# Kernel optimization log

Measured on AMD Instinct MI355X. Metric: run time of the kernel, lower is better.

## Reference

```python
import jax, jax.numpy as jnp
import numpy as np
from jax.ops import segment_sum, segment_max, segment_min

N_NODES = 200000
N_HE = 100000     # number of hyperedges (nets)
NNZ = 1000000     # number of pins (node,hyperedge) incidences
F_RAW = 29        # raw node features; +2 fake_pos +1 ismacro = 32 = num_features
PIN_D = 4
C = 64            # nhid (heads = 1)
N_MACRO = 512
NUM_CLASSES = 1
SLOPE = 0.1


def _lrelu(v):
    return jnp.where(v >= 0, v, SLOPE * v)


def setup_inputs() -> dict:
    key = jax.random.key(0)
    ks = jax.random.split(key, 16)
    x = jax.random.normal(ks[0], (N_NODES, F_RAW), jnp.float32)
    fake_pos = jax.random.uniform(ks[1], (N_NODES, 2), dtype=jnp.float32)
    node_idx = jax.random.randint(ks[2], (NNZ,), 0, N_NODES)
    he_idx = jax.random.randint(ks[3], (NNZ,), 0, N_HE)
    edge_index = jnp.stack([node_idx, he_idx]).astype(jnp.int32)
    pin_feature = jax.random.normal(ks[4], (NNZ, PIN_D), jnp.float32)
    macro_index = jax.random.randint(ks[5], (N_MACRO,), 0, N_NODES).astype(jnp.int32)
    F_IN = F_RAW + 3

    def lin(k, fi, fo):
        return (jax.random.normal(k, (fi, fo), jnp.float32) / np.float32(np.sqrt(fi)))

    W1 = lin(ks[6], F_IN, C); b1 = jnp.zeros((C,), jnp.float32)
    Wpin = lin(ks[7], PIN_D, C)
    att = jax.random.normal(ks[8], (2 * C,), jnp.float32) / np.float32(np.sqrt(2 * C))
    Wpost = lin(ks[9], 4 * C, C); bpost = jnp.zeros((C,), jnp.float32)
    Wm1 = lin(ks[10], 2 * C, C); bm1 = jnp.zeros((C,), jnp.float32)
    Wm2 = lin(ks[11], C, C // 2); bm2 = jnp.zeros((C // 2,), jnp.float32)
    Wm3 = lin(ks[12], C // 2, NUM_CLASSES); bm3 = jnp.zeros((NUM_CLASSES,), jnp.float32)
    return dict(x=x, fake_pos=fake_pos, edge_index=edge_index, pin_feature=pin_feature,
                macro_index=macro_index, W1=W1, b1=b1, Wpin=Wpin, att=att,
                Wpost=Wpost, bpost=bpost, Wm1=Wm1, bm1=bm1, Wm2=Wm2, bm2=bm2,
                Wm3=Wm3, bm3=bm3)


def _forward(x, fake_pos, edge_index, pin_feature, macro_index,
             W1, b1, Wpin, att, Wpost, bpost, Wm1, bm1, Wm2, bm2, Wm3, bm3):
    node_idx = edge_index[0]
    he_idx = edge_index[1]

    ismacro = jnp.zeros((N_NODES, 1), x.dtype).at[macro_index].set(1.0)
    h = jnp.concatenate([x, fake_pos, ismacro], axis=-1)  # (N, 32)

    xl = h @ W1 + b1                                      # (N, C) node embedding
    pin_m = pin_feature @ Wpin                            # (NNZ, C) pin embedding

    # node -> hyperedge aggregation (mean over incident pins)
    msg_ne = xl[node_idx] + pin_m                         # (NNZ, C)
    deg_e = segment_sum(jnp.ones((NNZ,), x.dtype), he_idx, num_segments=N_HE)
    e_feat = segment_sum(msg_ne, he_idx, num_segments=N_HE) / jnp.maximum(deg_e, 1.0)[:, None]

    # attention over incident hyperedges, softmax per node
    e_g = e_feat[he_idx]                                  # (NNZ, C)
    a_raw = _lrelu(jnp.concatenate([xl[node_idx], e_g], axis=-1) @ att)  # (NNZ,)
    m = segment_max(a_raw, node_idx, num_segments=N_NODES)
    m = jnp.where(jnp.isfinite(m), m, 0.0)
    ex = jnp.exp(a_raw - m[node_idx])
    den = segment_sum(ex, node_idx, num_segments=N_NODES)
    alpha = ex / (den[node_idx] + 1e-16)

    # hyperedge -> node: PNA multi-aggregation of attention-weighted messages
    msg = e_g * alpha[:, None]                            # (NNZ, C)
    deg_n = segment_sum(jnp.ones((NNZ,), x.dtype), node_idx, num_segments=N_NODES)
    deg_c = jnp.maximum(deg_n, 1.0)[:, None]
    s = segment_sum(msg, node_idx, num_segments=N_NODES)
    mean = s / deg_c
    mx = segment_max(msg, node_idx, num_segments=N_NODES)
    mx = jnp.where(deg_n[:, None] > 0, mx, 0.0)
    mn = segment_min(msg, node_idx, num_segments=N_NODES)
    mn = jnp.where(deg_n[:, None] > 0, mn, 0.0)
    sq = segment_sum(msg * msg, node_idx, num_segments=N_NODES) / deg_c
    std = jnp.sqrt(jnp.maximum(sq - mean * mean, 0.0) + 1e-12)

    pna = jnp.concatenate([mean, mx, mn, std], axis=-1) @ Wpost + bpost  # (N, C)
    hx = _lrelu(pna)

    # masked global-mean pools (single graph: batch is all zeros)
    pooled = jnp.concatenate([hx[macro_index].mean(0), hx.mean(0)])[None, :]  # (1, 2C)

    z = _lrelu(pooled @ Wm1 + bm1)
    z = _lrelu(z @ Wm2 + bm2)
    return z @ Wm3 + bm3                                  # (1, num_classes)


def reference(x, fake_pos, edge_index, pin_feature, macro_index,
              W1, b1, Wpin, att, Wpost, bpost, Wm1, bm1, Wm2, bm2, Wm3, bm3):
    return _forward(x, fake_pos, edge_index, pin_feature, macro_index,
                    W1, b1, Wpin, att, Wpost, bpost, Wm1, bm1, Wm2, bm2, Wm3, bm3)
```

## Files before the change

### kernel.cpp

```cpp
#include <hip/hip_runtime.h>
#include <math.h>

#define N_NODES 200000
#define N_HE    100000
#define NNZ     1000000
#define F_RAW   29
#define N_MACRO 512
#define SLOPE   0.1f
#define L_TOTAL (N_NODES + N_HE)
#define NB_SCAN 293

typedef __attribute__((ext_vector_type(8))) short bf16x8;
typedef __attribute__((ext_vector_type(4))) float f32x4;

__device__ __forceinline__ float lrelu(float v) { return v >= 0.f ? v : SLOPE * v; }
__device__ __forceinline__ float bf2f(unsigned short u) { return __uint_as_float(((unsigned)u) << 16); }
__device__ __forceinline__ unsigned short f2bf(float f) {
    unsigned u = __float_as_uint(f);
    unsigned r = u + 0x7FFFu + ((u >> 16) & 1u);
    return (unsigned short)(r >> 16);
}
__device__ __forceinline__ float bflo(unsigned u) { return __uint_as_float(u << 16); }
__device__ __forceinline__ float bfhi(unsigned u) { return __uint_as_float(u & 0xffff0000u); }

__global__ __launch_bounds__(256) void fill_f32(float* p, long long n, float v) {
    long long i = (long long)blockIdx.x * blockDim.x + threadIdx.x;
    long long st = (long long)gridDim.x * blockDim.x;
    for (; i < n; i += st) p[i] = v;
}

__global__ __launch_bounds__(256) void k_ismacro(const int* __restrict__ mi,
                                                 float* __restrict__ ismacro, int* __restrict__ mcount) {
    int i = blockIdx.x * blockDim.x + threadIdx.x;
    if (i < N_MACRO) {
        ismacro[mi[i]] = 1.0f;
        atomicAdd(&mcount[mi[i]], 1);
    }
}

__global__ __launch_bounds__(64) void k_va(const float* __restrict__ W1, const float* __restrict__ b1,
                                           const float* __restrict__ att, float* __restrict__ va) {
    int t = threadIdx.x;
    if (t < 32) {
        float a = 0.f;
        for (int c = 0; c < 64; c++) a += W1[t * 64 + c] * att[c];
        va[t] = a;
    } else if (t == 32) {
        float a = 0.f;
        for (int c = 0; c < 64; c++) a += b1[c] * att[c];
        va[32] = a;
    }
}

__global__ __launch_bounds__(256) void k_h(
    const float* __restrict__ x, const float* __restrict__ fp,
    const float* __restrict__ ismacro, const float* __restrict__ va,
    unsigned short* __restrict__ h, float* __restrict__ xn_att)
{
    const int lane = threadIdx.x & 63;
    const int half = lane >> 5, k = lane & 31;
    int wid = (blockIdx.x * blockDim.x + threadIdx.x) >> 6;
    int nw = (gridDim.x * blockDim.x) >> 6;
    float vak = va[k];
    float c0 = va[32];
    for (int base = wid * 2; base < N_NODES; base += nw * 2) {
        int n = base + half;
        float v;
        if (k < 29)       v = x[(size_t)n * F_RAW + k];
        else if (k == 29) v = fp[2 * n];
        else if (k == 30) v = fp[2 * n + 1];
        else              v = ismacro[n];
        h[(size_t)n * 32 + k] = f2bf(v);
        float r = v * vak;
        #pragma unroll
        for (int o = 16; o > 0; o >>= 1) r += __shfl_xor(r, o, 32);
        if (k == 0) xn_att[n] = r + c0;
    }
}

__global__ __launch_bounds__(256) void k_count(
    const int* __restrict__ nidx, const int* __restrict__ hidx,
    int* __restrict__ cnt, int* __restrict__ rank_n, int* __restrict__ rank_e)
{
    int i = blockIdx.x * blockDim.x + threadIdx.x;
    int st = gridDim.x * blockDim.x;
    for (int p = i; p < NNZ; p += st) {
        rank_n[p] = atomicAdd(&cnt[nidx[p]], 1);
        rank_e[p] = atomicAdd(&cnt[N_NODES + hidx[p]], 1);
    }
}

__global__ __launch_bounds__(256) void k_scan1(const int* __restrict__ cnt,
                                               int* __restrict__ row_ptr, int* __restrict__ partials)
{
    __shared__ int sA[256], sB[256];
    const int t = threadIdx.x;
    const int base = blockIdx.x * 1024 + t * 4;
    int v0 = base + 0 < L_TOTAL ? cnt[base + 0] : 0;
    int v1 = base + 1 < L_TOTAL ? cnt[base + 1] : 0;
    int v2 = base + 2 < L_TOTAL ? cnt[base + 2] : 0;
    int v3 = base + 3 < L_TOTAL ? cnt[base + 3] : 0;
    sA[t] = v0 + v1 + v2 + v3;
    __syncthreads();
    int* src = sA; int* dst = sB;
    for (int off = 1; off < 256; off <<= 1) {
        int v = src[t];
        if (t >= off) v += src[t - off];
        dst[t] = v;
        __syncthreads();
        int* tmp = src; src = dst; dst = tmp;
    }
    int excl = t > 0 ? src[t - 1] : 0;
    if (base + 0 < L_TOTAL) row_ptr[base + 0] = excl;
    if (base + 1 < L_TOTAL) row_ptr[base + 1] = excl + v0;
    if (base + 2 < L_TOTAL) row_ptr[base + 2] = excl + v0 + v1;
    if (base + 3 < L_TOTAL) row_ptr[base + 3] = excl + v0 + v1 + v2;
    if (t == 255) partials[blockIdx.x] = src[255];
}

__global__ __launch_bounds__(512) void k_scan2(int* __restrict__ partials)
{
    __shared__ int sA[512], sB[512];
    const int t = threadIdx.x;
    sA[t] = t < NB_SCAN ? partials[t] : 0;
    __syncthreads();
    int* src = sA; int* dst = sB;
    for (int off = 1; off < 512; off <<= 1) {
        int v = src[t];
        if (t >= off) v += src[t - off];
        dst[t] = v;
        __syncthreads();
        int* tmp = src; src = dst; dst = tmp;
    }
    if (t < NB_SCAN) partials[t] = t > 0 ? src[t - 1] : 0;
    if (t == 0) partials[NB_SCAN] = src[511];
}

__global__ __launch_bounds__(256) void k_scan3(int* __restrict__ row_ptr, const int* __restrict__ partials)
{
    const int base = blockIdx.x * 1024 + threadIdx.x * 4;
    int add = partials[blockIdx.x];
    #pragma unroll
    for (int k = 0; k < 4; k++)
        if (base + k < L_TOTAL) row_ptr[base + k] += add;
    if (blockIdx.x == 0 && threadIdx.x == 0) row_ptr[L_TOTAL] = partials[NB_SCAN];
}

__global__ __launch_bounds__(256) void k_scatter(
    const int* __restrict__ nidx, const int* __restrict__ hidx,
    const int* __restrict__ row_ptr,
    const int* __restrict__ rank_n, const int* __restrict__ rank_e,
    const float4* __restrict__ pf4, int* __restrict__ csr, ushort4* __restrict__ pfh)
{
    int i = blockIdx.x * blockDim.x + threadIdx.x;
    int st = gridDim.x * blockDim.x;
    for (int p = i; p < NNZ; p += st) {
        int n = nidx[p], e = hidx[p];
        csr[row_ptr[n] + rank_n[p]] = e;
        int pe = row_ptr[N_NODES + e] + rank_e[p];
        csr[pe] = n;
        float4 q = pf4[p];
        ushort4 r;
        r.x = f2bf(q.x); r.y = f2bf(q.y); r.z = f2bf(q.z); r.w = f2bf(q.w);
        pfh[pe - NNZ] = r;
    }
}

__global__ __launch_bounds__(256) void k_he_agg(
    const int* __restrict__ row_ptr, const int* __restrict__ csr,
    const ushort4* __restrict__ pfh,
    const float* __restrict__ W1, const float* __restrict__ Wpin,
    const float* __restrict__ b1, const float* __restrict__ att,
    const unsigned short* __restrict__ h,
    unsigned short* __restrict__ e_feat, float* __restrict__ e_att)
{
    __shared__ float sW1[32 * 64];
    __shared__ float sWp[4 * 64];
    __shared__ float sb1[64];
    for (int i = threadIdx.x; i < 32 * 64; i += 256) sW1[i] = W1[i];
    for (int i = threadIdx.x; i < 4 * 64; i += 256) sWp[i] = Wpin[i];
    if (threadIdx.x < 64) sb1[threadIdx.x] = b1[threadIdx.x];
    __syncthreads();
    const int lane = threadIdx.x & 63;
    const int g  = lane >> 4;
    const int gl = lane & 15;
    float att2 = att[64 + lane];
    int wid = (blockIdx.x * blockDim.x + threadIdx.x) >> 6;
    int nw = (gridDim.x * blockDim.x) >> 6;
    for (int e = wid; e < N_HE; e += nw) {
        int start = row_ptr[N_NODES + e];
        int deg = row_ptr[N_NODES + e + 1] - start;
        float hx = 0.f, hy = 0.f;
        {
            int t = g;
            for (; t + 4 < deg; t += 8) {
                int n0 = csr[start + t];
                int n1 = csr[start + t + 4];
                unsigned u0 = ((const unsigned*)&h[(size_t)n0 * 32])[gl];
                unsigned u1 = ((const unsigned*)&h[(size_t)n1 * 32])[gl];
                hx += bflo(u0) + bflo(u1);
                hy += bfhi(u0) + bfhi(u1);
            }
            for (; t < deg; t += 4) {
                int n = csr[start + t];
                unsigned u = ((const unsigned*)&h[(size_t)n * 32])[gl];
                hx += bflo(u); hy += bfhi(u);
            }
        }
        hx += __shfl_xor(hx, 16); hy += __shfl_xor(hy, 16);
        hx += __shfl_xor(hx, 32); hy += __shfl_xor(hy, 32);
        float p0 = 0.f, p1 = 0.f, p2 = 0.f, p3 = 0.f;
        for (int t = lane; t < deg; t += 64) {
            ushort4 r = pfh[start - NNZ + t];
            p0 += bf2f(r.x); p1 += bf2f(r.y); p2 += bf2f(r.z); p3 += bf2f(r.w);
        }
        #pragma unroll
        for (int o = 32; o > 0; o >>= 1) {
            p0 += __shfl_xor(p0, o, 64); p1 += __shfl_xor(p1, o, 64);
            p2 += __shfl_xor(p2, o, 64); p3 += __shfl_xor(p3, o, 64);
        }
        float acc = (float)deg * sb1[lane]
                  + p0 * sWp[lane] + p1 * sWp[64 + lane]
                  + p2 * sWp[128 + lane] + p3 * sWp[192 + lane];
        #pragma unroll
        for (int kk = 0; kk < 16; kk++) {
            float hvx = __shfl(hx, kk, 64);
            float hvy = __shfl(hy, kk, 64);
            acc += hvx * sW1[(2 * kk) * 64 + lane] + hvy * sW1[(2 * kk + 1) * 64 + lane];
        }
        float d = (float)(deg > 0 ? deg : 1);
        float v = acc / d;
        e_feat[(size_t)e * 64 + lane] = f2bf(v);
        float r = v * att2;
        #pragma unroll
        for (int o = 32; o > 0; o >>= 1) r += __shfl_down(r, o, 64);
        if (lane == 0) e_att[e] = r;
    }
}

__global__ __launch_bounds__(256, 4) void k_fused(
    const int* __restrict__ row_ptr, const int* __restrict__ csr,
    const float* __restrict__ xn_att, const float* __restrict__ e_att,
    const unsigned short* __restrict__ e_feat,
    const float* __restrict__ Wpost, const float* __restrict__ bpost,
    const int* __restrict__ mcount,
    float* __restrict__ sum_all, float* __restrict__ sum_mac)
{
    __shared__ __align__(16) unsigned short scat[16 * 264];
    const int lane = threadIdx.x & 63;
    const int wave = threadIdx.x >> 6;
    const int half = lane >> 5;
    const int c2   = lane & 31;
    const int quad = lane >> 4;
    const int nn   = lane & 15;
    bf16x8 wfrag[8];
    #pragma unroll
    for (int s = 0; s < 8; s++) {
        bf16x8 w;
        #pragma unroll
        for (int j = 0; j < 8; j++)
            w[j] = (short)f2bf(Wpost[(size_t)(32 * s + quad * 8 + j) * 64 + wave * 16 + nn]);
        wfrag[s] = w;
    }
    float bias = bpost[wave * 16 + nn];
    float pool = 0.f, pmac = 0.f;
    const int nbatches = N_NODES / 16;
    for (int b = blockIdx.x; b < nbatches; b += gridDim.x) {
        const int base = b * 16;
        __syncthreads();
        for (int i = 0; i < 4; i++) {
            int j = wave * 4 + i;
            int n = base + j;
            int start = row_ptr[n];
            int deg = row_ptr[n + 1] - start;
            float xn = xn_att[n];
            float sw = 0.f;
            float sx = 0.f, sy = 0.f, qx = 0.f, qy = 0.f;
            float mxx = -INFINITY, mxy = -INFINITY, mnx = INFINITY, mny = INFINITY;
            int t = half;
            for (; t + 2 < deg; t += 4) {
                int e0 = csr[start + t];
                int e1 = csr[start + t + 2];
                float w0 = __expf(lrelu(xn + e_att[e0]));
                float w1 = __expf(lrelu(xn + e_att[e1]));
                unsigned u0 = ((const unsigned*)&e_feat[(size_t)e0 * 64])[c2];
                unsigned u1 = ((const unsigned*)&e_feat[(size_t)e1 * 64])[c2];
                float v0x = bflo(u0) * w0, v0y = bfhi(u0) * w0;
                float v1x = bflo(u1) * w1, v1y = bfhi(u1) * w1;
                sw += w0 + w1;
                sx += v0x + v1x; sy += v0y + v1y;
                qx += v0x * v0x + v1x * v1x; qy += v0y * v0y + v1y * v1y;
                mxx = fmaxf(mxx, fmaxf(v0x, v1x)); mxy = fmaxf(mxy, fmaxf(v0y, v1y));
                mnx = fminf(mnx, fminf(v0x, v1x)); mny = fminf(mny, fminf(v0y, v1y));
            }
            for (; t < deg; t += 2) {
                int e = csr[start + t];
                float w = __expf(lrelu(xn + e_att[e]));
                unsigned u = ((const unsigned*)&e_feat[(size_t)e * 64])[c2];
                float vx = bflo(u) * w, vy = bfhi(u) * w;
                sw += w; sx += vx; sy += vy; qx += vx * vx; qy += vy * vy;
                mxx = fmaxf(mxx, vx); mxy = fmaxf(mxy, vy);
                mnx = fminf(mnx, vx); mny = fminf(mny, vy);
            }
            sw  += __shfl_xor(sw, 32);
            sx  += __shfl_xor(sx, 32);  sy += __shfl_xor(sy, 32);
            qx  += __shfl_xor(qx, 32);  qy += __shfl_xor(qy, 32);
            mxx = fmaxf(mxx, __shfl_xor(mxx, 32)); mxy = fmaxf(mxy, __shfl_xor(mxy, 32));
            mnx = fminf(mnx, __shfl_xor(mnx, 32)); mny = fminf(mny, __shfl_xor(mny, 32));
            float invD = 1.f / (sw + 1e-16f);
            float dc = (float)(deg > 0 ? deg : 1);
            float meanx = sx * invD / dc, meany = sy * invD / dc;
            float sqmx = qx * invD * invD / dc, sqmy = qy * invD * invD / dc;
            float stdx = sqrtf(fmaxf(sqmx - meanx * meanx, 0.f) + 1e-12f);
            float stdy = sqrtf(fmaxf(sqmy - meany * meany, 0.f) + 1e-12f);
            ushort2* row = (ushort2*)&scat[j * 264];
            if (half == 0) {
                ushort2 a; a.x = f2bf(meanx); a.y = f2bf(meany);
                row[c2] = a;
                ushort2 bmax; bmax.x = f2bf(deg > 0 ? mxx * invD : 0.f);
                bmax.y = f2bf(deg > 0 ? mxy * invD : 0.f);
                row[32 + c2] = bmax;
            } else {
                ushort2 bmin; bmin.x = f2bf(deg > 0 ? mnx * invD : 0.f);
                bmin.y = f2bf(deg > 0 ? mny * invD : 0.f);
                row[64 + c2] = bmin;
                ushort2 bstd; bstd.x = f2bf(stdx); bstd.y = f2bf(stdy);
                row[96 + c2] = bstd;
            }
        }
        __syncthreads();
        f32x4 acc = {0.f, 0.f, 0.f, 0.f};
        #pragma unroll
        for (int s = 0; s < 8; s++) {
            bf16x8 a = *(const bf16x8*)&scat[nn * 264 + 32 * s + quad * 8];
            acc = __builtin_amdgcn_mfma_f32_16x16x32_bf16(a, wfrag[s], acc, 0, 0, 0);
        }
        int4 mc4 = *(const int4*)&mcount[base + 4 * quad];
        float h0 = lrelu(acc[0] + bias);
        float h1 = lrelu(acc[1] + bias);
        float h2 = lrelu(acc[2] + bias);
        float h3 = lrelu(acc[3] + bias);
        pool += h0 + h1 + h2 + h3;
        pmac += (float)mc4.x * h0 + (float)mc4.y * h1 + (float)mc4.z * h2 + (float)mc4.w * h3;
    }
    pool += __shfl_xor(pool, 16); pool += __shfl_xor(pool, 32);
    pmac += __shfl_xor(pmac, 16); pmac += __shfl_xor(pmac, 32);
    if (quad == 0) {
        atomicAdd(&sum_all[wave * 16 + nn], pool);
        atomicAdd(&sum_mac[wave * 16 + nn], pmac);
    }
}

__global__ __launch_bounds__(256) void k_final(
    const float* __restrict__ sum_all, const float* __restrict__ sum_mac,
    const float* __restrict__ Wm1, const float* __restrict__ bm1,
    const float* __restrict__ Wm2, const float* __restrict__ bm2,
    const float* __restrict__ Wm3, const float* __restrict__ bm3,
    float* __restrict__ out)
{
    __shared__ float spool[128];
    __shared__ float z1[64];
    __shared__ float z2[32];
    if (threadIdx.x < 64) {
        spool[threadIdx.x]      = sum_mac[threadIdx.x] / (float)N_MACRO;
        spool[64 + threadIdx.x] = sum_all[threadIdx.x] / (float)N_NODES;
    }
    __syncthreads();
    if (threadIdx.x < 64) {
        int j = threadIdx.x;
        float a = bm1[j];
        #pragma unroll 4
        for (int k = 0; k < 128; k++) a += spool[k] * Wm1[k * 64 + j];
        z1[j] = lrelu(a);
    }
    __syncthreads();
    if (threadIdx.x < 32) {
        int j = threadIdx.x;
        float a = bm2[j];
        #pragma unroll 4
        for (int k = 0; k < 64; k++) a += z1[k] * Wm2[k * 32 + j];
        z2[j] = lrelu(a);
    }
    __syncthreads();
    if (threadIdx.x == 0) {
        float a = bm3[0];
        #pragma unroll
        for (int k = 0; k < 32; k++) a += z2[k] * Wm3[k];
        out[0] = a;
    }
}

extern "C" void kernel_launch(void* const* d_in, const int* in_sizes, int n_in,
                              void* d_out, int out_size, void* d_ws, size_t ws_size,
                              hipStream_t stream)
{
    const float* x        = (const float*)d_in[0];
    const float* fake_pos = (const float*)d_in[1];
    const int*   edge     = (const int*)d_in[2];
    const float* pinf     = (const float*)d_in[3];
    const int*   macro    = (const int*)d_in[4];
    const float* W1    = (const float*)d_in[5];
    const float* b1    = (const float*)d_in[6];
    const float* Wpin  = (const float*)d_in[7];
    const float* att   = (const float*)d_in[8];
    const float* Wpost = (const float*)d_in[9];
    const float* bpost = (const float*)d_in[10];
    const float* Wm1   = (const float*)d_in[11];
    const float* bm1   = (const float*)d_in[12];
    const float* Wm2   = (const float*)d_in[13];
    const float* bm2   = (const float*)d_in[14];
    const float* Wm3   = (const float*)d_in[15];
    const float* bm3   = (const float*)d_in[16];
    float* out = (float*)d_out;

    float* ws = (float*)d_ws;
    float*    ismacro = ws;
    float*    sum_all = ws + 200000;
    float*    sum_mac = ws + 200064;
    int*      mcount  = (int*)(ws + 200128);
    int*      cnt     = (int*)(ws + 400128);
    int*      row_ptr  = (int*)(ws + 700128);
    int*      partials = (int*)(ws + 1000132);
    float*    va       = ws + 1000432;
    int*      rank_n   = (int*)(ws + 1000472);
    int*      rank_e   = (int*)(ws + 2000472);
    int*      csr      = (int*)(ws + 3000472);
    ushort4*  pfh      = (ushort4*)(ws + 5000472);
    float*    e_att    = ws + 7000472;
    float*    xn_att   = ws + 7100472;
    unsigned short* h      = (unsigned short*)(ws + 7300472);
    unsigned short* e_feat = (unsigned short*)(ws + 10500472);

    const int* nidx = edge;
    const int* hidx = edge + NNZ;

    fill_f32<<<1024, 256, 0, stream>>>(ws, 700128LL, 0.f);
    k_ismacro<<<2, 256, 0, stream>>>(macro, ismacro, mcount);
    k_count<<<2048, 256, 0, stream>>>(nidx, hidx, cnt, rank_n, rank_e);
    k_va<<<1, 64, 0, stream>>>(W1, b1, att, va);
    k_h<<<2048, 256, 0, stream>>>(x, fake_pos, ismacro, va, h, xn_att);
    k_scan1<<<NB_SCAN, 256, 0, stream>>>(cnt, row_ptr, partials);
    k_scan2<<<1, 512, 0, stream>>>(partials);
    k_scan3<<<NB_SCAN, 256, 0, stream>>>(row_ptr, partials);
    k_scatter<<<2048, 256, 0, stream>>>(nidx, hidx, row_ptr, rank_n, rank_e,
                                        (const float4*)pinf, csr, pfh);
    k_he_agg<<<2048, 256, 0, stream>>>(row_ptr, csr, pfh, W1, Wpin, b1, att, h, e_feat, e_att);
    k_fused<<<2048, 256, 0, stream>>>(row_ptr, csr, xn_att, e_att, e_feat, Wpost, bpost,
                                      mcount, sum_all, sum_mac);
    k_final<<<1, 256, 0, stream>>>(sum_all, sum_mac, Wm1, bm1, Wm2, bm2, Wm3, bm3, out);
}
```

Baseline: 499.3 us.

## Merge small setup kernels and pack hyperedge pin records with node ids

```diff
diff --git a/kernel.cpp b/kernel.cpp
--- a/kernel.cpp
+++ b/kernel.cpp
@@ -29,64 +29,37 @@
     for (; i < n; i += st) p[i] = v;
 }
 
-__global__ __launch_bounds__(256) void k_ismacro(const int* __restrict__ mi,
-                                                 float* __restrict__ ismacro, int* __restrict__ mcount) {
-    int i = blockIdx.x * blockDim.x + threadIdx.x;
-    if (i < N_MACRO) {
-        ismacro[mi[i]] = 1.0f;
-        atomicAdd(&mcount[mi[i]], 1);
-    }
-}
-
-__global__ __launch_bounds__(64) void k_va(const float* __restrict__ W1, const float* __restrict__ b1,
-                                           const float* __restrict__ att, float* __restrict__ va) {
-    int t = threadIdx.x;
-    if (t < 32) {
-        float a = 0.f;
-        for (int c = 0; c < 64; c++) a += W1[t * 64 + c] * att[c];
-        va[t] = a;
-    } else if (t == 32) {
-        float a = 0.f;
-        for (int c = 0; c < 64; c++) a += b1[c] * att[c];
-        va[32] = a;
-    }
-}
-
-__global__ __launch_bounds__(256) void k_h(
-    const float* __restrict__ x, const float* __restrict__ fp,
-    const float* __restrict__ ismacro, const float* __restrict__ va,
-    unsigned short* __restrict__ h, float* __restrict__ xn_att)
-{
-    const int lane = threadIdx.x & 63;
-    const int half = lane >> 5, k = lane & 31;
-    int wid = (blockIdx.x * blockDim.x + threadIdx.x) >> 6;
-    int nw = (gridDim.x * blockDim.x) >> 6;
-    float vak = va[k];
-    float c0 = va[32];
-    for (int base = wid * 2; base < N_NODES; base += nw * 2) {
-        int n = base + half;
-        float v;
-        if (k < 29)       v = x[(size_t)n * F_RAW + k];
-        else if (k == 29) v = fp[2 * n];
-        else if (k == 30) v = fp[2 * n + 1];
-        else              v = ismacro[n];
-        h[(size_t)n * 32 + k] = f2bf(v);
-        float r = v * vak;
-        #pragma unroll
-        for (int o = 16; o > 0; o >>= 1) r += __shfl_xor(r, o, 32);
-        if (k == 0) xn_att[n] = r + c0;
-    }
-}
-
-__global__ __launch_bounds__(256) void k_count(
+__global__ __launch_bounds__(256) void k_pre(
+    const int* __restrict__ mi, float* __restrict__ ismacro, int* __restrict__ mcount,
+    const float* __restrict__ W1, const float* __restrict__ b1,
+    const float* __restrict__ att, float* __restrict__ va,
     const int* __restrict__ nidx, const int* __restrict__ hidx,
     int* __restrict__ cnt, int* __restrict__ rank_n, int* __restrict__ rank_e)
 {
-    int i = blockIdx.x * blockDim.x + threadIdx.x;
-    int st = gridDim.x * blockDim.x;
-    for (int p = i; p < NNZ; p += st) {
-        rank_n[p] = atomicAdd(&cnt[nidx[p]], 1);
-        rank_e[p] = atomicAdd(&cnt[N_NODES + hidx[p]], 1);
+    if (blockIdx.x == 0) {
+        int t = threadIdx.x;
+        if (t < 32) {
+            float a = 0.f;
+            for (int c = 0; c < 64; c++) a += W1[t * 64 + c] * att[c];
+            va[t] = a;
+        } else if (t == 32) {
+            float a = 0.f;
+            for (int c = 0; c < 64; c++) a += b1[c] * att[c];
+            va[32] = a;
+        }
+    } else if (blockIdx.x <= 2) {
+        int i = (blockIdx.x - 1) * 256 + threadIdx.x;
+        if (i < N_MACRO) {
+            ismacro[mi[i]] = 1.0f;
+            atomicAdd(&mcount[mi[i]], 1);
+        }
+    } else {
+        int i = (blockIdx.x - 3) * 256 + threadIdx.x;
+        int st = (gridDim.x - 3) * 256;
+        for (int p = i; p < NNZ; p += st) {
+            rank_n[p] = atomicAdd(&cnt[nidx[p]], 1);
+            rank_e[p] = atomicAdd(&cnt[N_NODES + hidx[p]], 1);
+        }
     }
 }
 
@@ -146,29 +119,55 @@
     if (blockIdx.x == 0 && threadIdx.x == 0) row_ptr[L_TOTAL] = partials[NB_SCAN];
 }
 
-__global__ __launch_bounds__(256) void k_scatter(
+__global__ __launch_bounds__(256) void k_mid(
     const int* __restrict__ nidx, const int* __restrict__ hidx,
     const int* __restrict__ row_ptr,
     const int* __restrict__ rank_n, const int* __restrict__ rank_e,
-    const float4* __restrict__ pf4, int* __restrict__ csr, ushort4* __restrict__ pfh)
-{
-    int i = blockIdx.x * blockDim.x + threadIdx.x;
-    int st = gridDim.x * blockDim.x;
-    for (int p = i; p < NNZ; p += st) {
-        int n = nidx[p], e = hidx[p];
-        csr[row_ptr[n] + rank_n[p]] = e;
-        int pe = row_ptr[N_NODES + e] + rank_e[p];
-        csr[pe] = n;
-        float4 q = pf4[p];
-        ushort4 r;
-        r.x = f2bf(q.x); r.y = f2bf(q.y); r.z = f2bf(q.z); r.w = f2bf(q.w);
-        pfh[pe - NNZ] = r;
+    const float4* __restrict__ pf4, int* __restrict__ csr_n, int4* __restrict__ rec,
+    const float* __restrict__ x, const float* __restrict__ fp,
+    const float* __restrict__ ismacro, const float* __restrict__ va,
+    unsigned short* __restrict__ h, float* __restrict__ xn_att)
+{
+    if (blockIdx.x < 2048) {
+        int i = blockIdx.x * 256 + threadIdx.x;
+        int st = 2048 * 256;
+        for (int p = i; p < NNZ; p += st) {
+            int n = nidx[p], e = hidx[p];
+            csr_n[row_ptr[n] + rank_n[p]] = e;
+            int pe = row_ptr[N_NODES + e] + rank_e[p];
+            float4 q = pf4[p];
+            int4 r;
+            r.x = n;
+            r.y = (int)((unsigned)f2bf(q.x) | ((unsigned)f2bf(q.y) << 16));
+            r.z = (int)((unsigned)f2bf(q.z) | ((unsigned)f2bf(q.w) << 16));
+            r.w = 0;
+            rec[pe - NNZ] = r;
+        }
+    } else {
+        const int lane = threadIdx.x & 63;
+        const int half = lane >> 5, k = lane & 31;
+        int wid = ((blockIdx.x - 2048) * 256 + threadIdx.x) >> 6;
+        int nw = (1024 * 256) >> 6;
+        float vak = va[k];
+        float c0 = va[32];
+        for (int base = wid * 2; base < N_NODES; base += nw * 2) {
+            int n = base + half;
+            float v;
+            if (k < 29)       v = x[(size_t)n * F_RAW + k];
+            else if (k == 29) v = fp[2 * n];
+            else if (k == 30) v = fp[2 * n + 1];
+            else              v = ismacro[n];
+            h[(size_t)n * 32 + k] = f2bf(v);
+            float r = v * vak;
+            #pragma unroll
+            for (int o = 16; o > 0; o >>= 1) r += __shfl_xor(r, o, 32);
+            if (k == 0) xn_att[n] = r + c0;
+        }
     }
 }
 
 __global__ __launch_bounds__(256) void k_he_agg(
-    const int* __restrict__ row_ptr, const int* __restrict__ csr,
-    const ushort4* __restrict__ pfh,
+    const int* __restrict__ row_ptr, const int4* __restrict__ rec,
     const float* __restrict__ W1, const float* __restrict__ Wpin,
     const float* __restrict__ b1, const float* __restrict__ att,
     const unsigned short* __restrict__ h,
@@ -182,51 +181,56 @@
     if (threadIdx.x < 64) sb1[threadIdx.x] = b1[threadIdx.x];
     __syncthreads();
     const int lane = threadIdx.x & 63;
-    const int g  = lane >> 4;
-    const int gl = lane & 15;
+    const int g  = lane >> 3;
+    const int gl = lane & 7;
     float att2 = att[64 + lane];
     int wid = (blockIdx.x * blockDim.x + threadIdx.x) >> 6;
     int nw = (gridDim.x * blockDim.x) >> 6;
     for (int e = wid; e < N_HE; e += nw) {
         int start = row_ptr[N_NODES + e];
         int deg = row_ptr[N_NODES + e + 1] - start;
-        float hx = 0.f, hy = 0.f;
-        {
-            int t = g;
-            for (; t + 4 < deg; t += 8) {
-                int n0 = csr[start + t];
-                int n1 = csr[start + t + 4];
-                unsigned u0 = ((const unsigned*)&h[(size_t)n0 * 32])[gl];
-                unsigned u1 = ((const unsigned*)&h[(size_t)n1 * 32])[gl];
-                hx += bflo(u0) + bflo(u1);
-                hy += bfhi(u0) + bfhi(u1);
-            }
-            for (; t < deg; t += 4) {
-                int n = csr[start + t];
-                unsigned u = ((const unsigned*)&h[(size_t)n * 32])[gl];
-                hx += bflo(u); hy += bfhi(u);
-            }
-        }
-        hx += __shfl_xor(hx, 16); hy += __shfl_xor(hy, 16);
-        hx += __shfl_xor(hx, 32); hy += __shfl_xor(hy, 32);
-        float p0 = 0.f, p1 = 0.f, p2 = 0.f, p3 = 0.f;
-        for (int t = lane; t < deg; t += 64) {
-            ushort4 r = pfh[start - NNZ + t];
-            p0 += bf2f(r.x); p1 += bf2f(r.y); p2 += bf2f(r.z); p3 += bf2f(r.w);
-        }
-        #pragma unroll
-        for (int o = 32; o > 0; o >>= 1) {
-            p0 += __shfl_xor(p0, o, 64); p1 += __shfl_xor(p1, o, 64);
-            p2 += __shfl_xor(p2, o, 64); p3 += __shfl_xor(p3, o, 64);
-        }
+        float h0 = 0.f, h1 = 0.f, h2 = 0.f, h3 = 0.f;
+        float pa = 0.f, pb = 0.f;
+        const int4* rbase = rec + (start - NNZ);
+        int t = g;
+        for (; t + 8 < deg; t += 16) {
+            int4 rA = rbase[t];
+            int4 rB = rbase[t + 8];
+            ushort4 uA = *(const ushort4*)&h[(size_t)rA.x * 32 + 4 * gl];
+            ushort4 uB = *(const ushort4*)&h[(size_t)rB.x * 32 + 4 * gl];
+            h0 += bf2f(uA.x) + bf2f(uB.x);
+            h1 += bf2f(uA.y) + bf2f(uB.y);
+            h2 += bf2f(uA.z) + bf2f(uB.z);
+            h3 += bf2f(uA.w) + bf2f(uB.w);
+            unsigned pyA = (gl == 0) ? (unsigned)rA.y : ((gl == 1) ? (unsigned)rA.z : 0u);
+            unsigned pyB = (gl == 0) ? (unsigned)rB.y : ((gl == 1) ? (unsigned)rB.z : 0u);
+            pa += bflo(pyA) + bflo(pyB);
+            pb += bfhi(pyA) + bfhi(pyB);
+        }
+        if (t < deg) {
+            int4 r = rbase[t];
+            ushort4 u = *(const ushort4*)&h[(size_t)r.x * 32 + 4 * gl];
+            h0 += bf2f(u.x); h1 += bf2f(u.y); h2 += bf2f(u.z); h3 += bf2f(u.w);
+            unsigned py = (gl == 0) ? (unsigned)r.y : ((gl == 1) ? (unsigned)r.z : 0u);
+            pa += bflo(py); pb += bfhi(py);
+        }
+        #pragma unroll
+        for (int o = 8; o <= 32; o <<= 1) {
+            h0 += __shfl_xor(h0, o); h1 += __shfl_xor(h1, o);
+            h2 += __shfl_xor(h2, o); h3 += __shfl_xor(h3, o);
+            pa += __shfl_xor(pa, o); pb += __shfl_xor(pb, o);
+        }
+        float p0 = __shfl(pa, 0, 64), p1 = __shfl(pb, 0, 64);
+        float p2 = __shfl(pa, 1, 64), p3 = __shfl(pb, 1, 64);
         float acc = (float)deg * sb1[lane]
                   + p0 * sWp[lane] + p1 * sWp[64 + lane]
                   + p2 * sWp[128 + lane] + p3 * sWp[192 + lane];
         #pragma unroll
-        for (int kk = 0; kk < 16; kk++) {
-            float hvx = __shfl(hx, kk, 64);
-            float hvy = __shfl(hy, kk, 64);
-            acc += hvx * sW1[(2 * kk) * 64 + lane] + hvy * sW1[(2 * kk + 1) * 64 + lane];
+        for (int kk = 0; kk < 8; kk++) {
+            float a0 = __shfl(h0, kk, 64), a1 = __shfl(h1, kk, 64);
+            float a2 = __shfl(h2, kk, 64), a3 = __shfl(h3, kk, 64);
+            acc += a0 * sW1[(4 * kk + 0) * 64 + lane] + a1 * sW1[(4 * kk + 1) * 64 + lane]
+                 + a2 * sW1[(4 * kk + 2) * 64 + lane] + a3 * sW1[(4 * kk + 3) * 64 + lane];
         }
         float d = (float)(deg > 0 ? deg : 1);
         float v = acc / d;
@@ -424,28 +428,27 @@
     float*    va       = ws + 1000432;
     int*      rank_n   = (int*)(ws + 1000472);
     int*      rank_e   = (int*)(ws + 2000472);
-    int*      csr      = (int*)(ws + 3000472);
-    ushort4*  pfh      = (ushort4*)(ws + 5000472);
-    float*    e_att    = ws + 7000472;
-    float*    xn_att   = ws + 7100472;
-    unsigned short* h      = (unsigned short*)(ws + 7300472);
-    unsigned short* e_feat = (unsigned short*)(ws + 10500472);
+    int*      csr_n    = (int*)(ws + 3000472);
+    int4*     rec      = (int4*)(ws + 4000472);
+    float*    e_att    = ws + 8000472;
+    float*    xn_att   = ws + 8100472;
+    unsigned short* h      = (unsigned short*)(ws + 8300472);
+    unsigned short* e_feat = (unsigned short*)(ws + 11500472);
 
     const int* nidx = edge;
     const int* hidx = edge + NNZ;
 
     fill_f32<<<1024, 256, 0, stream>>>(ws, 700128LL, 0.f);
-    k_ismacro<<<2, 256, 0, stream>>>(macro, ismacro, mcount);
-    k_count<<<2048, 256, 0, stream>>>(nidx, hidx, cnt, rank_n, rank_e);
-    k_va<<<1, 64, 0, stream>>>(W1, b1, att, va);
-    k_h<<<2048, 256, 0, stream>>>(x, fake_pos, ismacro, va, h, xn_att);
+    k_pre<<<2051, 256, 0, stream>>>(macro, ismacro, mcount, W1, b1, att, va,
+                                    nidx, hidx, cnt, rank_n, rank_e);
     k_scan1<<<NB_SCAN, 256, 0, stream>>>(cnt, row_ptr, partials);
     k_scan2<<<1, 512, 0, stream>>>(partials);
     k_scan3<<<NB_SCAN, 256, 0, stream>>>(row_ptr, partials);
-    k_scatter<<<2048, 256, 0, stream>>>(nidx, hidx, row_ptr, rank_n, rank_e,
-                                        (const float4*)pinf, csr, pfh);
-    k_he_agg<<<2048, 256, 0, stream>>>(row_ptr, csr, pfh, W1, Wpin, b1, att, h, e_feat, e_att);
-    k_fused<<<2048, 256, 0, stream>>>(row_ptr, csr, xn_att, e_att, e_feat, Wpost, bpost,
+    k_mid<<<3072, 256, 0, stream>>>(nidx, hidx, row_ptr, rank_n, rank_e,
+                                    (const float4*)pinf, csr_n, rec,
+                                    x, fake_pos, ismacro, va, h, xn_att);
+    k_he_agg<<<2048, 256, 0, stream>>>(row_ptr, rec, W1, Wpin, b1, att, h, e_feat, e_att);
+    k_fused<<<2048, 256, 0, stream>>>(row_ptr, csr_n, xn_att, e_att, e_feat, Wpost, bpost,
                                       mcount, sum_all, sum_mac);
     k_final<<<1, 256, 0, stream>>>(sum_all, sum_mac, Wm1, bm1, Wm2, bm2, Wm3, bm3, out);
 }
```

New measurement: 474.0 us. -5.1%, faster.
